# Performance work log

Hardware: AMD Instinct MI355X
Metric: run time of the kernel (lower is better)

## Reference

```python
import jax, jax.numpy as jnp
import numpy as np

EPS = 1e-6

def _layer_norm(x, w, b):
    mu = jnp.mean(x, axis=-1, keepdims=True)
    var = jnp.mean((x - mu) ** 2, axis=-1, keepdims=True)
    return (x - mu) * jax.lax.rsqrt(var + EPS) * w + b

def setup_inputs() -> dict:
    key = jax.random.key(0)
    ks = jax.random.split(key, 8)
    B, N, C = 4, 1024, 2048
    H = C * 2  # mlp hidden = 2*feature_dim
    std = 0.01
    x = jax.random.normal(ks[0], (B, N, C), dtype=jnp.float32)
    wq = jax.random.normal(ks[1], (C, C), dtype=jnp.float32) * std
    wk = jax.random.normal(ks[2], (C, C), dtype=jnp.float32) * std
    wv = jax.random.normal(ks[3], (C, C), dtype=jnp.float32) * std
    ln1_w = jnp.ones((C,), jnp.float32); ln1_b = jnp.zeros((C,), jnp.float32)
    fc1_w = jax.random.normal(ks[4], (H, C), dtype=jnp.float32) * std
    fc1_b = jnp.zeros((H,), jnp.float32)
    fc2_w = jax.random.normal(ks[5], (C, H), dtype=jnp.float32) * std
    fc2_b = jnp.zeros((C,), jnp.float32)
    ln2_w = jnp.ones((C,), jnp.float32); ln2_b = jnp.zeros((C,), jnp.float32)
    return {"x": x, "wq": wq, "wk": wk, "wv": wv,
            "ln1_w": ln1_w, "ln1_b": ln1_b,
            "fc1_w": fc1_w, "fc1_b": fc1_b,
            "fc2_w": fc2_w, "fc2_b": fc2_b,
            "ln2_w": ln2_w, "ln2_b": ln2_b}

def reference(x, wq, wk, wv, ln1_w, ln1_b, fc1_w, fc1_b, fc2_w, fc2_b, ln2_w, ln2_b):
    B, N, C = x.shape
    num_head = 32
    d = C // num_head
    # QKV projections (no bias), split heads: [B, H, N, d]
    def proj(w):
        return (x @ w.T).reshape(B, N, num_head, d).transpose(0, 2, 1, 3)
    q, k, v = proj(wq), proj(wk), proj(wv)
    scale = 1.0 / jnp.sqrt(jnp.float32(d))
    attn = jnp.einsum('bhnd,bhmd->bhnm', q * scale, k)
    attn = jax.nn.softmax(attn, axis=-1)
    out = jnp.einsum('bhnm,bhmd->bhnd', attn, v)
    out = out.transpose(0, 2, 1, 3).reshape(B, N, C)
    out = _layer_norm(out + x, ln1_w, ln1_b)
    # MLP with residual + post-LN
    h = jax.nn.relu(out @ fc1_w.T + fc1_b)
    h = h @ fc2_w.T + fc2_b
    out = _layer_norm(out + h, ln2_w, ln2_b)
    return out
```

## Files before the change

### kernel.cpp

```cpp
#include <hip/hip_runtime.h>

#define C_DIM   2048
#define H_DIM   4096
#define NSEQ    1024
#define NBATCH  4
#define BN_ROWS 4096
#define NHEAD   32
#define DHEAD   64

typedef __attribute__((ext_vector_type(8))) short  short8;
typedef __attribute__((ext_vector_type(4))) float  f32x4;

__device__ __forceinline__ float bf2f(unsigned short u) {
    union { unsigned int i; float f; } v; v.i = ((unsigned int)u) << 16; return v.f;
}
__device__ __forceinline__ unsigned short f2bf(float f) {
    union { float f; unsigned int i; } v; v.f = f;
    unsigned int r = v.i + 0x7fffu + ((v.i >> 16) & 1u);
    return (unsigned short)(r >> 16);
}

#define G2L16(gp, lp) \
    __builtin_amdgcn_global_load_lds((const __attribute__((address_space(1))) void*)(gp), \
                                     (__attribute__((address_space(3))) void*)(lp), 16, 0, 0)

__global__ __launch_bounds__(256)
void cvt_all(const float* __restrict__ x,   unsigned short* __restrict__ xo,
             const float* __restrict__ w0,  unsigned short* __restrict__ w0o,
             const float* __restrict__ w1,  unsigned short* __restrict__ w1o,
             const float* __restrict__ w2,  unsigned short* __restrict__ w2o,
             const float* __restrict__ w3,  unsigned short* __restrict__ w3o,
             const float* __restrict__ w4,  unsigned short* __restrict__ w4o)
{
    int bid = blockIdx.x;
    const float* src; unsigned short* dst;
    if      (bid < 4096)  { src = x;  dst = xo;  }
    else if (bid < 6144)  { src = w0; dst = w0o; bid -= 4096;  }
    else if (bid < 8192)  { src = w1; dst = w1o; bid -= 6144;  }
    else if (bid < 10240) { src = w2; dst = w2o; bid -= 8192;  }
    else if (bid < 14336) { src = w3; dst = w3o; bid -= 10240; }
    else                  { src = w4; dst = w4o; bid -= 14336; }
    const size_t i = ((size_t)bid * 256 + threadIdx.x) * 8;
    float4 a = *(const float4*)(src + i);
    float4 b = *(const float4*)(src + i + 4);
    unsigned short o[8] = { f2bf(a.x), f2bf(a.y), f2bf(a.z), f2bf(a.w),
                            f2bf(b.x), f2bf(b.y), f2bf(b.z), f2bf(b.w) };
    *(int4*)(dst + i) = *(const int4*)o;
}

template<int EPI, typename OUT_T>
__global__ __launch_bounds__(256)
void gemm_bt(const unsigned short* __restrict__ A,
             const unsigned short* __restrict__ B,
             const float* __restrict__ bias,
             OUT_T* __restrict__ C, int M, int N, int K)
{
    __shared__ unsigned short As[128 * 32];
    __shared__ unsigned short Bs[128 * 32];

    const int t    = threadIdx.x;
    const int lane = t & 63;
    const int wave = t >> 6;
    const int m0 = blockIdx.x * 128, n0 = blockIdx.y * 128;
    const int wm = (wave >> 1) * 64, wn = (wave & 1) * 64;
    const int lr = lane & 15;
    const int kq = lane >> 4;

    f32x4 acc[4][4] = {};

    const int lrow = lane >> 2;
    const int lcol = (lane & 3) * 8;

    for (int kt = 0; kt < K; kt += 32) {
        __syncthreads();
        #pragma unroll
        for (int p = 0; p < 2; ++p) {
            const int rb = wave * 32 + p * 16;
            G2L16(&A[(size_t)(m0 + rb + lrow) * K + kt + lcol], &As[rb * 32]);
            G2L16(&B[(size_t)(n0 + rb + lrow) * K + kt + lcol], &Bs[rb * 32]);
        }
        __syncthreads();

        short8 af[4], bf[4];
        #pragma unroll
        for (int i = 0; i < 4; ++i)
            af[i] = *(const short8*)&As[(wm + i * 16 + lr) * 32 + kq * 8];
        #pragma unroll
        for (int j = 0; j < 4; ++j)
            bf[j] = *(const short8*)&Bs[(wn + j * 16 + lr) * 32 + kq * 8];
        #pragma unroll
        for (int i = 0; i < 4; ++i)
            #pragma unroll
            for (int j = 0; j < 4; ++j)
                acc[i][j] = __builtin_amdgcn_mfma_f32_16x16x32_bf16(af[i], bf[j], acc[i][j], 0, 0, 0);
    }

    #pragma unroll
    for (int j = 0; j < 4; ++j) {
        const int col = n0 + wn + j * 16 + lr;
        float bv = 0.f;
        if (EPI > 0) bv = bias[col];
        #pragma unroll
        for (int i = 0; i < 4; ++i) {
            #pragma unroll
            for (int r = 0; r < 4; ++r) {
                const int row = m0 + wm + i * 16 + kq * 4 + r;
                float v = acc[i][j][r] + bv;
                if (EPI == 1) v = fmaxf(v, 0.f);
                if constexpr (sizeof(OUT_T) == 2) C[(size_t)row * N + col] = f2bf(v);
                else                              C[(size_t)row * N + col] = v;
            }
        }
    }
}

__global__ __launch_bounds__(256)
void gemm_qkv(const unsigned short* __restrict__ A,
              const unsigned short* __restrict__ Wq,
              const unsigned short* __restrict__ Wk,
              const unsigned short* __restrict__ Wv,
              unsigned short* __restrict__ Qo,
              unsigned short* __restrict__ Ko,
              unsigned short* __restrict__ Vo)
{
    __shared__ unsigned short As[128 * 32];
    __shared__ unsigned short Bs[128 * 32];

    const int t    = threadIdx.x;
    const int lane = t & 63;
    const int wave = t >> 6;
    const int m0 = blockIdx.x * 128;
    const int ng = blockIdx.y * 128;
    const unsigned short* B; unsigned short* Cp; int n0;
    if      (ng < 2048) { B = Wq; Cp = Qo; n0 = ng; }
    else if (ng < 4096) { B = Wk; Cp = Ko; n0 = ng - 2048; }
    else                { B = Wv; Cp = Vo; n0 = ng - 4096; }

    const int wm = (wave >> 1) * 64, wn = (wave & 1) * 64;
    const int lr = lane & 15;
    const int kq = lane >> 4;

    f32x4 acc[4][4] = {};

    const int lrow = lane >> 2;
    const int lcol = (lane & 3) * 8;

    for (int kt = 0; kt < C_DIM; kt += 32) {
        __syncthreads();
        #pragma unroll
        for (int p = 0; p < 2; ++p) {
            const int rb = wave * 32 + p * 16;
            G2L16(&A[(size_t)(m0 + rb + lrow) * C_DIM + kt + lcol], &As[rb * 32]);
            G2L16(&B[(size_t)(n0 + rb + lrow) * C_DIM + kt + lcol], &Bs[rb * 32]);
        }
        __syncthreads();

        short8 af[4], bf[4];
        #pragma unroll
        for (int i = 0; i < 4; ++i)
            af[i] = *(const short8*)&As[(wm + i * 16 + lr) * 32 + kq * 8];
        #pragma unroll
        for (int j = 0; j < 4; ++j)
            bf[j] = *(const short8*)&Bs[(wn + j * 16 + lr) * 32 + kq * 8];
        #pragma unroll
        for (int i = 0; i < 4; ++i)
            #pragma unroll
            for (int j = 0; j < 4; ++j)
                acc[i][j] = __builtin_amdgcn_mfma_f32_16x16x32_bf16(af[i], bf[j], acc[i][j], 0, 0, 0);
    }

    #pragma unroll
    for (int j = 0; j < 4; ++j) {
        const int col = n0 + wn + j * 16 + lr;
        #pragma unroll
        for (int i = 0; i < 4; ++i) {
            #pragma unroll
            for (int r = 0; r < 4; ++r) {
                const int row = m0 + wm + i * 16 + kq * 4 + r;
                Cp[(size_t)row * C_DIM + col] = f2bf(acc[i][j][r]);
            }
        }
    }
}

#define LDK 72
__global__ __launch_bounds__(256)
void attn_mfma(const unsigned short* __restrict__ Qg,
               const unsigned short* __restrict__ Kg,
               const unsigned short* __restrict__ Vg,
               unsigned short* __restrict__ Og)
{
    __shared__ unsigned short Ks[64 * LDK];
    __shared__ unsigned short Vt[64 * LDK];
    __shared__ unsigned short Ps[64 * LDK];

    const int t    = threadIdx.x;
    const int lane = t & 63;
    const int wave = t >> 6;
    const int lr   = lane & 15;
    const int quad = lane >> 4;
    const int bh = blockIdx.y;
    const int b  = bh >> 5, h = bh & 31;
    const int q0 = blockIdx.x * 64;
    const int colbase = h * 64;

    short8 qf[2];
    {
        const size_t qrow = (size_t)(b * NSEQ + q0 + wave * 16 + lr) * C_DIM + colbase;
        #pragma unroll
        for (int kc = 0; kc < 2; ++kc) {
            short8 raw = *(const short8*)(Qg + qrow + kc * 32 + quad * 8);
            short8 sc;
            #pragma unroll
            for (int j = 0; j < 8; ++j)
                sc[j] = (short)f2bf(bf2f((unsigned short)raw[j]) * 0.125f);
            qf[kc] = sc;
        }
    }

    f32x4 Oacc[4] = {};
    float li[4] = {};

    for (int kt = 0; kt < 16; ++kt) {
        __syncthreads();
        {
            const int r = t >> 2, sg = (t & 3) * 16;
            const size_t grow = (size_t)(b * NSEQ + kt * 64 + r) * C_DIM + colbase + sg;
            *(int4*)&Ks[r * LDK + sg]     = *(const int4*)(Kg + grow);
            *(int4*)&Ks[r * LDK + sg + 8] = *(const int4*)(Kg + grow + 8);
        }
        {
            const int key = t & 63, d0 = (t >> 6) * 16;
            const size_t grow = (size_t)(b * NSEQ + kt * 64 + key) * C_DIM + colbase + d0;
            int4 u0 = *(const int4*)(Vg + grow);
            int4 u1 = *(const int4*)(Vg + grow + 8);
            const unsigned short* us0 = (const unsigned short*)&u0;
            const unsigned short* us1 = (const unsigned short*)&u1;
            #pragma unroll
            for (int j = 0; j < 8; ++j) {
                Vt[(d0 + j)     * LDK + key] = us0[j];
                Vt[(d0 + j + 8) * LDK + key] = us1[j];
            }
        }
        __syncthreads();

        f32x4 s[4] = {};
        #pragma unroll
        for (int n = 0; n < 4; ++n)
            #pragma unroll
            for (int kc = 0; kc < 2; ++kc) {
                short8 kf = *(const short8*)&Ks[(n * 16 + lr) * LDK + kc * 32 + quad * 8];
                s[n] = __builtin_amdgcn_mfma_f32_16x16x32_bf16(qf[kc], kf, s[n], 0, 0, 0);
            }

        float p[4][4];
        #pragma unroll
        for (int r = 0; r < 4; ++r) {
            #pragma unroll
            for (int n = 0; n < 4; ++n) { p[n][r] = __expf(s[n][r]); }
            li[r] += p[0][r] + p[1][r] + p[2][r] + p[3][r];
        }

        #pragma unroll
        for (int r = 0; r < 4; ++r)
            #pragma unroll
            for (int n = 0; n < 4; ++n)
                Ps[(wave * 16 + quad * 4 + r) * LDK + n * 16 + lr] = f2bf(p[n][r]);

        short8 pf[2];
        #pragma unroll
        for (int kc = 0; kc < 2; ++kc)
            pf[kc] = *(const short8*)&Ps[(wave * 16 + lr) * LDK + kc * 32 + quad * 8];

        #pragma unroll
        for (int n = 0; n < 4; ++n)
            #pragma unroll
            for (int kc = 0; kc < 2; ++kc) {
                short8 vf = *(const short8*)&Vt[(n * 16 + lr) * LDK + kc * 32 + quad * 8];
                Oacc[n] = __builtin_amdgcn_mfma_f32_16x16x32_bf16(pf[kc], vf, Oacc[n], 0, 0, 0);
            }
    }

    #pragma unroll
    for (int r = 0; r < 4; ++r) {
        #pragma unroll
        for (int off = 1; off < 16; off <<= 1) li[r] += __shfl_xor(li[r], off, 64);
        const float inv = 1.f / li[r];
        const size_t rowb = (size_t)(b * NSEQ + q0 + wave * 16 + quad * 4 + r) * C_DIM + colbase;
        #pragma unroll
        for (int n = 0; n < 4; ++n)
            Og[rowb + n * 16 + lr] = f2bf(Oacc[n][r] * inv);
    }
}

__global__ __launch_bounds__(256)
void ln_fused1(const unsigned short* __restrict__ a, const float* __restrict__ xr,
               const float* __restrict__ w, const float* __restrict__ bb,
               unsigned short* __restrict__ y16)
{
    const int row = blockIdx.x, t = threadIdx.x;
    const size_t base = (size_t)row * C_DIM;
    const int c0 = t * 8;
    float v[8];
    int4 ai = *(const int4*)(a + base + c0);
    const unsigned short* as = (const unsigned short*)&ai;
    float4 x0 = *(const float4*)(xr + base + c0);
    float4 x1 = *(const float4*)(xr + base + c0 + 4);
    v[0] = bf2f(as[0]) + x0.x; v[1] = bf2f(as[1]) + x0.y;
    v[2] = bf2f(as[2]) + x0.z; v[3] = bf2f(as[3]) + x0.w;
    v[4] = bf2f(as[4]) + x1.x; v[5] = bf2f(as[5]) + x1.y;
    v[6] = bf2f(as[6]) + x1.z; v[7] = bf2f(as[7]) + x1.w;

    float s = 0.f, s2 = 0.f;
    #pragma unroll
    for (int k = 0; k < 8; ++k) { s += v[k]; s2 += v[k] * v[k]; }
    #pragma unroll
    for (int off = 32; off; off >>= 1) { s += __shfl_xor(s, off, 64); s2 += __shfl_xor(s2, off, 64); }
    __shared__ float red[8];
    if ((t & 63) == 0) { red[t >> 6] = s; red[4 + (t >> 6)] = s2; }
    __syncthreads();
    s  = red[0] + red[1] + red[2] + red[3];
    s2 = red[4] + red[5] + red[6] + red[7];
    const float mu = s * (1.f / C_DIM);
    const float rs = rsqrtf(s2 * (1.f / C_DIM) - mu * mu + 1e-6f);

    float4 w0 = *(const float4*)(w + c0);
    float4 w1 = *(const float4*)(w + c0 + 4);
    float4 b0 = *(const float4*)(bb + c0);
    float4 b1 = *(const float4*)(bb + c0 + 4);
    const float* wf = (const float*)&w0; const float* wg = (const float*)&w1;
    const float* bf = (const float*)&b0; const float* bg = (const float*)&b1;
    unsigned short o16[8];
    #pragma unroll
    for (int k = 0; k < 4; ++k) {
        o16[k]     = f2bf((v[k]     - mu) * rs * wf[k] + bf[k]);
        o16[k + 4] = f2bf((v[k + 4] - mu) * rs * wg[k] + bg[k]);
    }
    *(int4*)(y16 + base + c0) = *(const int4*)o16;
}

__global__ __launch_bounds__(256)
void ln_fused2(const unsigned short* __restrict__ a, const unsigned short* __restrict__ b2,
               const float* __restrict__ w, const float* __restrict__ bb,
               float* __restrict__ out)
{
    const int row = blockIdx.x, t = threadIdx.x;
    const size_t base = (size_t)row * C_DIM;
    const int c0 = t * 8;
    float v[8];
    int4 ai = *(const int4*)(a + base + c0);
    int4 bi = *(const int4*)(b2 + base + c0);
    const unsigned short* as = (const unsigned short*)&ai;
    const unsigned short* bs = (const unsigned short*)&bi;
    #pragma unroll
    for (int k = 0; k < 8; ++k) v[k] = bf2f(as[k]) + bf2f(bs[k]);

    float s = 0.f, s2 = 0.f;
    #pragma unroll
    for (int k = 0; k < 8; ++k) { s += v[k]; s2 += v[k] * v[k]; }
    #pragma unroll
    for (int off = 32; off; off >>= 1) { s += __shfl_xor(s, off, 64); s2 += __shfl_xor(s2, off, 64); }
    __shared__ float red[8];
    if ((t & 63) == 0) { red[t >> 6] = s; red[4 + (t >> 6)] = s2; }
    __syncthreads();
    s  = red[0] + red[1] + red[2] + red[3];
    s2 = red[4] + red[5] + red[6] + red[7];
    const float mu = s * (1.f / C_DIM);
    const float rs = rsqrtf(s2 * (1.f / C_DIM) - mu * mu + 1e-6f);

    float4 w0 = *(const float4*)(w + c0);
    float4 w1 = *(const float4*)(w + c0 + 4);
    float4 b0 = *(const float4*)(bb + c0);
    float4 b1 = *(const float4*)(bb + c0 + 4);
    const float* wf = (const float*)&w0; const float* wg = (const float*)&w1;
    const float* bf = (const float*)&b0; const float* bg = (const float*)&b1;
    float4 o0, o1;
    #pragma unroll
    for (int k = 0; k < 4; ++k) {
        ((float*)&o0)[k] = (v[k]     - mu) * rs * wf[k] + bf[k];
        ((float*)&o1)[k] = (v[k + 4] - mu) * rs * wg[k] + bg[k];
    }
    *(float4*)(out + base + c0)     = o0;
    *(float4*)(out + base + c0 + 4) = o1;
}

extern "C" void kernel_launch(void* const* d_in, const int* in_sizes, int n_in,
                              void* d_out, int out_size, void* d_ws, size_t ws_size,
                              hipStream_t stream)
{
    (void)in_sizes; (void)n_in; (void)out_size; (void)ws_size;
    const float* x    = (const float*)d_in[0];
    const float* wq   = (const float*)d_in[1];
    const float* wk   = (const float*)d_in[2];
    const float* wv   = (const float*)d_in[3];
    const float* ln1w = (const float*)d_in[4];
    const float* ln1b = (const float*)d_in[5];
    const float* fc1w = (const float*)d_in[6];
    const float* fc1b = (const float*)d_in[7];
    const float* fc2w = (const float*)d_in[8];
    const float* fc2b = (const float*)d_in[9];
    const float* ln2w = (const float*)d_in[10];
    const float* ln2b = (const float*)d_in[11];

    char* ws = (char*)d_ws;
    const size_t MB16 = (size_t)BN_ROWS * C_DIM * 2;
    unsigned short* xb    = (unsigned short*)(ws);
    unsigned short* attnb = (unsigned short*)(ws);
    unsigned short* wqb   = (unsigned short*)(ws + MB16);
    unsigned short* wkb   = (unsigned short*)(ws + MB16 + MB16 / 2);
    unsigned short* y16   = (unsigned short*)(ws + MB16);
    unsigned short* wvb   = (unsigned short*)(ws + 2 * MB16);
    unsigned short* fc1wb = (unsigned short*)(ws + 2 * MB16 + MB16 / 2);
    unsigned short* fc2wb = (unsigned short*)(ws + 3 * MB16 + MB16 / 2);
    unsigned short* q_ws  = (unsigned short*)(ws + 4 * MB16 + MB16 / 2);
    unsigned short* h2    = (unsigned short*)(ws + 4 * MB16 + MB16 / 2);
    unsigned short* k_ws  = (unsigned short*)(ws + 5 * MB16 + MB16 / 2);
    unsigned short* v_ws  = (unsigned short*)(ws + 6 * MB16 + MB16 / 2);
    unsigned short* hbuf  = (unsigned short*)(ws + 5 * MB16 + MB16 / 2);

    dim3 blk(256);

    cvt_all<<<dim3(18432), blk, 0, stream>>>(x, xb, wq, wqb, wk, wkb, wv, wvb,
                                             fc1w, fc1wb, fc2w, fc2wb);

    gemm_qkv<<<dim3(32, 48), blk, 0, stream>>>(xb, wqb, wkb, wvb, q_ws, k_ws, v_ws);
    attn_mfma<<<dim3(NSEQ / 64, NBATCH * NHEAD), blk, 0, stream>>>(q_ws, k_ws, v_ws, attnb);
    ln_fused1<<<dim3(BN_ROWS), blk, 0, stream>>>(attnb, x, ln1w, ln1b, y16);
    gemm_bt<1, unsigned short><<<dim3(32, 32), blk, 0, stream>>>(y16, fc1wb, fc1b, hbuf, BN_ROWS, H_DIM, C_DIM);
    gemm_bt<2, unsigned short><<<dim3(32, 16), blk, 0, stream>>>(hbuf, fc2wb, fc2b, h2, BN_ROWS, C_DIM, H_DIM);
    ln_fused2<<<dim3(BN_ROWS), blk, 0, stream>>>(y16, h2, ln2w, ln2b, (float*)d_out);
}
```

Baseline: 607.2 us.

## Pipeline GEMM global-to-LDS loads with a four-slot ring buffer

Both the QKV GEMM and the MLP GEMMs now keep a 4-slot LDS ring. Loads run three k-tiles ahead, and the code waits with explicit vmcnt counters and a single barrier per iteration, replacing the two syncthreads around each load. This is meant to hide global memory latency behind MFMA work. LDS use rises to 64KB per block, which may lower occupancy. Reusing a slot right after a single barrier relies on the vmcnt counting being correct.

Result: faster. 580.9 us (-4.3%).

```diff
diff --git a/kernel.cpp b/kernel.cpp
--- a/kernel.cpp
+++ b/kernel.cpp
@@ -50,13 +50,13 @@
 
 template<int EPI, typename OUT_T>
 __global__ __launch_bounds__(256)
-void gemm_bt(const unsigned short* __restrict__ A,
-             const unsigned short* __restrict__ B,
-             const float* __restrict__ bias,
-             OUT_T* __restrict__ C, int M, int N, int K)
-{
-    __shared__ unsigned short As[128 * 32];
-    __shared__ unsigned short Bs[128 * 32];
+void gemm_ring(const unsigned short* __restrict__ A,
+               const unsigned short* __restrict__ B,
+               const float* __restrict__ bias,
+               OUT_T* __restrict__ C, int M, int N, int K)
+{
+    __shared__ unsigned short As[4][128 * 32];
+    __shared__ unsigned short Bs[4][128 * 32];
 
     const int t    = threadIdx.x;
     const int lane = t & 63;
@@ -65,34 +65,49 @@
     const int wm = (wave >> 1) * 64, wn = (wave & 1) * 64;
     const int lr = lane & 15;
     const int kq = lane >> 4;
-
-    f32x4 acc[4][4] = {};
-
     const int lrow = lane >> 2;
     const int lcol = (lane & 3) * 8;
-
-    for (int kt = 0; kt < K; kt += 32) {
-        __syncthreads();
-        #pragma unroll
-        for (int p = 0; p < 2; ++p) {
-            const int rb = wave * 32 + p * 16;
-            G2L16(&A[(size_t)(m0 + rb + lrow) * K + kt + lcol], &As[rb * 32]);
-            G2L16(&B[(size_t)(n0 + rb + lrow) * K + kt + lcol], &Bs[rb * 32]);
-        }
-        __syncthreads();
-
+    const int NT = K >> 5;
+
+    const int arow = m0 + wave * 32 + lrow;
+    const int brow = n0 + wave * 32 + lrow;
+    const int rb   = wave * 32;
+
+    f32x4 acc[4][4] = {};
+
+#define STAGE_T(slot, ktile) do {                                              \
+    const int koff_ = (ktile) * 32 + lcol;                                     \
+    G2L16(&A[(size_t)(arow)      * K + koff_], &As[slot][ rb       * 32]);     \
+    G2L16(&A[(size_t)(arow + 16) * K + koff_], &As[slot][(rb + 16) * 32]);     \
+    G2L16(&B[(size_t)(brow)      * K + koff_], &Bs[slot][ rb       * 32]);     \
+    G2L16(&B[(size_t)(brow + 16) * K + koff_], &Bs[slot][(rb + 16) * 32]);     \
+  } while (0)
+
+    STAGE_T(0, 0);
+    STAGE_T(1, 1);
+    STAGE_T(2, 2);
+
+    for (int kt = 0; kt < NT; ++kt) {
+        if (kt < NT - 2)       asm volatile("s_waitcnt vmcnt(8)" ::: "memory");
+        else if (kt == NT - 2) asm volatile("s_waitcnt vmcnt(4)" ::: "memory");
+        else                   asm volatile("s_waitcnt vmcnt(0)" ::: "memory");
+        __builtin_amdgcn_s_barrier();
+
+        const int s = kt & 3;
         short8 af[4], bf[4];
         #pragma unroll
         for (int i = 0; i < 4; ++i)
-            af[i] = *(const short8*)&As[(wm + i * 16 + lr) * 32 + kq * 8];
+            af[i] = *(const short8*)&As[s][(wm + i * 16 + lr) * 32 + kq * 8];
         #pragma unroll
         for (int j = 0; j < 4; ++j)
-            bf[j] = *(const short8*)&Bs[(wn + j * 16 + lr) * 32 + kq * 8];
+            bf[j] = *(const short8*)&Bs[s][(wn + j * 16 + lr) * 32 + kq * 8];
         #pragma unroll
         for (int i = 0; i < 4; ++i)
             #pragma unroll
             for (int j = 0; j < 4; ++j)
                 acc[i][j] = __builtin_amdgcn_mfma_f32_16x16x32_bf16(af[i], bf[j], acc[i][j], 0, 0, 0);
+
+        if (kt + 3 < NT) STAGE_T((kt + 3) & 3, kt + 3);
     }
 
     #pragma unroll
@@ -112,6 +127,7 @@
             }
         }
     }
+#undef STAGE_T
 }
 
 __global__ __launch_bounds__(256)
@@ -123,8 +139,8 @@
               unsigned short* __restrict__ Ko,
               unsigned short* __restrict__ Vo)
 {
-    __shared__ unsigned short As[128 * 32];
-    __shared__ unsigned short Bs[128 * 32];
+    __shared__ unsigned short As[4][128 * 32];
+    __shared__ unsigned short Bs[4][128 * 32];
 
     const int t    = threadIdx.x;
     const int lane = t & 63;
@@ -139,34 +155,49 @@
     const int wm = (wave >> 1) * 64, wn = (wave & 1) * 64;
     const int lr = lane & 15;
     const int kq = lane >> 4;
-
-    f32x4 acc[4][4] = {};
-
     const int lrow = lane >> 2;
     const int lcol = (lane & 3) * 8;
-
-    for (int kt = 0; kt < C_DIM; kt += 32) {
-        __syncthreads();
-        #pragma unroll
-        for (int p = 0; p < 2; ++p) {
-            const int rb = wave * 32 + p * 16;
-            G2L16(&A[(size_t)(m0 + rb + lrow) * C_DIM + kt + lcol], &As[rb * 32]);
-            G2L16(&B[(size_t)(n0 + rb + lrow) * C_DIM + kt + lcol], &Bs[rb * 32]);
-        }
-        __syncthreads();
-
+    const int NT = C_DIM >> 5;
+
+    const int arow = m0 + wave * 32 + lrow;
+    const int brow = n0 + wave * 32 + lrow;
+    const int rb   = wave * 32;
+
+    f32x4 acc[4][4] = {};
+
+#define STAGE_T(slot, ktile) do {                                                   \
+    const int koff_ = (ktile) * 32 + lcol;                                          \
+    G2L16(&A[(size_t)(arow)      * C_DIM + koff_], &As[slot][ rb       * 32]);      \
+    G2L16(&A[(size_t)(arow + 16) * C_DIM + koff_], &As[slot][(rb + 16) * 32]);      \
+    G2L16(&B[(size_t)(brow)      * C_DIM + koff_], &Bs[slot][ rb       * 32]);      \
+    G2L16(&B[(size_t)(brow + 16) * C_DIM + koff_], &Bs[slot][(rb + 16) * 32]);      \
+  } while (0)
+
+    STAGE_T(0, 0);
+    STAGE_T(1, 1);
+    STAGE_T(2, 2);
+
+    for (int kt = 0; kt < NT; ++kt) {
+        if (kt < NT - 2)       asm volatile("s_waitcnt vmcnt(8)" ::: "memory");
+        else if (kt == NT - 2) asm volatile("s_waitcnt vmcnt(4)" ::: "memory");
+        else                   asm volatile("s_waitcnt vmcnt(0)" ::: "memory");
+        __builtin_amdgcn_s_barrier();
+
+        const int s = kt & 3;
         short8 af[4], bf[4];
         #pragma unroll
         for (int i = 0; i < 4; ++i)
-            af[i] = *(const short8*)&As[(wm + i * 16 + lr) * 32 + kq * 8];
+            af[i] = *(const short8*)&As[s][(wm + i * 16 + lr) * 32 + kq * 8];
         #pragma unroll
         for (int j = 0; j < 4; ++j)
-            bf[j] = *(const short8*)&Bs[(wn + j * 16 + lr) * 32 + kq * 8];
+            bf[j] = *(const short8*)&Bs[s][(wn + j * 16 + lr) * 32 + kq * 8];
         #pragma unroll
         for (int i = 0; i < 4; ++i)
             #pragma unroll
             for (int j = 0; j < 4; ++j)
                 acc[i][j] = __builtin_amdgcn_mfma_f32_16x16x32_bf16(af[i], bf[j], acc[i][j], 0, 0, 0);
+
+        if (kt + 3 < NT) STAGE_T((kt + 3) & 3, kt + 3);
     }
 
     #pragma unroll
@@ -181,6 +212,7 @@
             }
         }
     }
+#undef STAGE_T
 }
 
 #define LDK 72
@@ -426,7 +458,7 @@
     gemm_qkv<<<dim3(32, 48), blk, 0, stream>>>(xb, wqb, wkb, wvb, q_ws, k_ws, v_ws);
     attn_mfma<<<dim3(NSEQ / 64, NBATCH * NHEAD), blk, 0, stream>>>(q_ws, k_ws, v_ws, attnb);
     ln_fused1<<<dim3(BN_ROWS), blk, 0, stream>>>(attnb, x, ln1w, ln1b, y16);
-    gemm_bt<1, unsigned short><<<dim3(32, 32), blk, 0, stream>>>(y16, fc1wb, fc1b, hbuf, BN_ROWS, H_DIM, C_DIM);
-    gemm_bt<2, unsigned short><<<dim3(32, 16), blk, 0, stream>>>(hbuf, fc2wb, fc2b, h2, BN_ROWS, C_DIM, H_DIM);
+    gemm_ring<1, unsigned short><<<dim3(32, 32), blk, 0, stream>>>(y16, fc1wb, fc1b, hbuf, BN_ROWS, H_DIM, C_DIM);
+    gemm_ring<2, unsigned short><<<dim3(32, 16), blk, 0, stream>>>(hbuf, fc2wb, fc2b, h2, BN_ROWS, C_DIM, H_DIM);
     ln_fused2<<<dim3(BN_ROWS), blk, 0, stream>>>(y16, h2, ln2w, ln2b, (float*)d_out);
 }
```
